# Performance work log

Measured on AMD Instinct MI355X. Metric: run time of the kernel, lower is better.

The kernel has to match this reference:

```python
import jax, jax.numpy as jnp
import numpy as np

# ---- config (matches init_kwargs) ----
GROUP_NUM = 2048
K_NEIGHBORS = 32
OUT_DIM = 192
SIGMA, BASELINE, SCALING, EPS = 0.26, 0.1, 10.0, 1e-6
ALPHA, BETA = 1000.0, 100.0
ADAPTIVE_RATIO = 0.5
IN_DIM = 3
ADAPTIVE_DIM = int(OUT_DIM * ADAPTIVE_RATIO)          # 96
FOURIER_DIM = OUT_DIM - ADAPTIVE_DIM                  # 96
FEAT_DIM_F = FOURIER_DIM // (IN_DIM * 2)              # 16
FEAT_DIM_A = int(np.ceil(ADAPTIVE_DIM / IN_DIM))      # 32
FEAT_NUM_A = FEAT_DIM_A * IN_DIM                      # 96
OUT_IDX = np.linspace(0, FEAT_NUM_A - 1, ADAPTIVE_DIM).astype(np.int64)


def setup_inputs() -> dict:
    key = jax.random.key(0)
    k1, k2, k3, k4 = jax.random.split(key, 4)
    xyz = jax.random.normal(k1, (4, 8192, 3), dtype=jnp.float32)
    x = jax.random.normal(k2, (4, 8192, 96), dtype=jnp.float32)
    bn_gamma = jax.random.uniform(k3, (192,), dtype=jnp.float32)
    bn_beta = jax.random.normal(k4, (192,), dtype=jnp.float32)
    return {"xyz": xyz, "x": x, "bn_gamma": bn_gamma, "bn_beta": bn_beta}


def _fps(xyz, m):
    """Farthest point sampling. xyz: [B,N,3] -> idx [B,m] (int32). Seed = index 0."""
    def single(pts):
        n = pts.shape[0]
        def step(carry, _):
            dists, last = carry
            d = jnp.sum((pts - pts[last]) ** 2, axis=-1)
            dists = jnp.minimum(dists, d)
            nxt = jnp.argmax(dists).astype(jnp.int32)
            return (dists, nxt), nxt
        init = (jnp.full((n,), 1e10, pts.dtype), jnp.array(0, jnp.int32))
        _, idxs = jax.lax.scan(step, init, None, length=m - 1)
        return jnp.concatenate([jnp.zeros((1,), jnp.int32), idxs])
    return jax.vmap(single)(xyz)


def _square_distance(src, dst):
    # src: [B,S,3], dst: [B,N,3] -> [B,S,N]
    d = -2.0 * jnp.einsum('bsc,bnc->bsn', src, dst)
    d += jnp.sum(src ** 2, -1)[:, :, None]
    d += jnp.sum(dst ** 2, -1)[:, None, :]
    return d


def _gather_knn(points, idx):
    # points: [B,N,C], idx: [B,G,K] -> [B,G,K,C]
    return jax.vmap(lambda p, i: p[i])(points, idx)


def _forward(xyz, x, bn_gamma, bn_beta):
    B, N, _ = xyz.shape
    G, K = GROUP_NUM, K_NEIGHBORS

    # ---- Grouper_seg ----
    fps_idx = _fps(xyz, G)                                   # [B,G]
    lc_xyz = jnp.take_along_axis(xyz, fps_idx[..., None], 1)  # [B,G,3]
    lc_x = jnp.take_along_axis(x, fps_idx[..., None], 1)      # [B,G,C]
    sqr = _square_distance(lc_xyz, xyz)                       # [B,G,N]
    knn_idx = jax.lax.top_k(-sqr, K)[1]                       # [B,G,K] smallest-k
    knn_xyz = _gather_knn(xyz, knn_idx)                       # [B,G,K,3]
    knn_x = _gather_knn(x, knn_idx)                           # [B,G,K,C]

    # ---- Aggregation_seg: local normalization ----
    mean_x = lc_x[:, :, None, :]
    std_x = jnp.std(knn_x - mean_x, ddof=1)
    mean_xyz = lc_xyz[:, :, None, :]
    std_xyz = jnp.std(knn_xyz - mean_xyz, ddof=1)
    knn_x = (knn_x - mean_x) / (std_x + 1e-5)
    knn_xyz_n = (knn_xyz - mean_xyz) / (std_xyz + 1e-5)       # [B,G,K,3]
    C = knn_x.shape[-1]
    knn_x = jnp.concatenate(
        [knn_x, jnp.broadcast_to(lc_x[:, :, None, :], (B, G, K, C))], axis=-1)  # [B,G,K,2C]
    knn_xyz_cf = jnp.transpose(knn_xyz_n, (0, 3, 1, 2))       # [B,3,G,K]
    knn_x_cf = jnp.transpose(knn_x, (0, 3, 1, 2))             # [B,OUT_DIM,G,K]

    # ---- PosE_Geo: fourier part ----
    feat_range = jnp.arange(FEAT_DIM_F, dtype=knn_xyz_cf.dtype)
    dim_embed = ALPHA ** (feat_range / FEAT_DIM_F)            # [F]
    div = BETA * knn_xyz_cf[..., None] / dim_embed            # [B,3,G,K,F]
    fourier = jnp.stack([jnp.sin(div), jnp.cos(div)], axis=-1)  # [B,3,G,K,F,2]
    fourier = fourier.reshape(B, IN_DIM, G, K, 2 * FEAT_DIM_F)
    fourier = jnp.transpose(fourier, (0, 1, 4, 2, 3)).reshape(B, FOURIER_DIM, G, K)

    # ---- AdaptiveEmbedding (parameterless, data-driven) ----
    x4 = knn_xyz_n                                            # [B,G,K,3]
    gstd = jnp.mean(jnp.std(x4.reshape(B, -1, IN_DIM), axis=1, ddof=1))
    sig = SIGMA * (1.0 + gstd) + EPS
    blend = jax.nn.sigmoid((gstd - BASELINE) * SCALING)
    feat_val = jnp.linspace(-1.0, 1.0, FEAT_DIM_A + 2)[1:-1]  # [Fa]
    z = (x4[..., None] - feat_val) / sig                      # [B,G,K,3,Fa]
    comb = blend * jnp.exp(-0.5 * z * z) + (1.0 - blend) * jnp.cos(z)
    ae = comb.reshape(B, G, K, FEAT_NUM_A)[..., OUT_IDX]      # [B,G,K,ADAPTIVE_DIM]
    ae_cf = jnp.transpose(ae, (0, 3, 1, 2))                   # [B,ADAPTIVE_DIM,G,K]

    pe = jnp.concatenate([fourier, ae_cf], axis=1)            # [B,OUT_DIM,G,K]
    knn_x_w = (knn_x_cf + pe) * pe

    # ---- Pooling_seg: max+mean pool, BatchNorm1d (train stats) + GELU ----
    lc = jnp.max(knn_x_w, -1) + jnp.mean(knn_x_w, -1)         # [B,OUT_DIM,G]
    mu = jnp.mean(lc, axis=(0, 2), keepdims=True)
    var = jnp.var(lc, axis=(0, 2), keepdims=True)
    y = (lc - mu) / jnp.sqrt(var + 1e-5)
    y = y * bn_gamma[None, :, None] + bn_beta[None, :, None]
    return jax.nn.gelu(y, approximate=False)


def reference(xyz, x, bn_gamma, bn_beta):
    return _forward(xyz, x, bn_gamma, bn_beta)
```

## Files before the change

kernel.cpp:

```cpp
#include <hip/hip_runtime.h>
#include <cstdint>
#include <math.h>

#define NPTS 8192
#define NB 4
#define NG 2048
#define NK 32
#define CIN 96
#define COUT 192

typedef float v2f __attribute__((ext_vector_type(2)));

__global__ __launch_bounds__(256) void setup_kernel(const float* __restrict__ xyz,
                                                    float* __restrict__ xs, float* __restrict__ ys,
                                                    float* __restrict__ zs, float* __restrict__ d2){
  int i = blockIdx.x*256 + threadIdx.x;
  if (i >= NB*NPTS) return;
  float x = xyz[3*i+0], y = xyz[3*i+1], z = xyz[3*i+2];
  xs[i]=x; ys[i]=y; zs[i]=z;
  d2[i] = __fadd_rn(__fadd_rn(__fmul_rn(x,x),__fmul_rn(y,y)),__fmul_rn(z,z));
}

__global__ __launch_bounds__(256,1) void fps_kernel(const float* __restrict__ xyz, int* __restrict__ fps_idx){
#pragma clang fp contract(off)
  extern __shared__ char smem[];
  float4* ctab = (float4*)smem;
  unsigned long long* slots = (unsigned long long*)(smem + NPTS*16);
  const int b = blockIdx.x;
  const int t = threadIdx.x;
  const float* base = xyz + (size_t)b*NPTS*3;
  v2f px[16], py[16], pz[16], D[16];
#pragma unroll
  for (int j=0;j<16;++j){
    int p0 = t + 512*j, p1 = p0 + 256;
    float x0=base[3*p0+0], y0=base[3*p0+1], z0=base[3*p0+2];
    float x1=base[3*p1+0], y1=base[3*p1+1], z1=base[3*p1+2];
    px[j]=(v2f){x0,x1}; py[j]=(v2f){y0,y1}; pz[j]=(v2f){z0,z1};
    D[j]=(v2f){1e10f,1e10f};
    ctab[p0] = make_float4(x0,y0,z0,0.f);
    ctab[p1] = make_float4(x1,y1,z1,0.f);
  }
  if (t<4) slots[t]=0ULL;
  if (t==0) fps_idx[b*NG]=0;
  __syncthreads();
  float lx=base[0], ly=base[1], lz=base[2];
  for (int it=0; it<NG-1; ++it){
    v2f bm = (v2f){-1.0f,-1.0f};
#pragma unroll
    for (int j=0;j<16;++j){
      v2f dx = px[j]-lx, dy = py[j]-ly, dz = pz[j]-lz;
      v2f s = (dx*dx + dy*dy) + dz*dz;
      v2f nd = __builtin_elementwise_min(D[j], s);
      D[j] = nd;
      bm = __builtin_elementwise_max(bm, nd);
    }
    float bd = fmaxf(bm.x, bm.y);
    int bj = 0;
#pragma unroll
    for (int j=15;j>=0;--j){
      if (D[j].y == bd) bj = 2*j+1;
      if (D[j].x == bd) bj = 2*j;
    }
    const int bp = t + (bj<<8);
    unsigned long long key = (((unsigned long long)__float_as_uint(bd))<<32)
                           | (unsigned long long)(unsigned)(~bp);
#pragma unroll
    for (int off=32; off>0; off>>=1){
      unsigned long long ok = __shfl_xor(key, off);
      if (ok > key) key = ok;
    }
    if ((t&63)==0) atomicMax(&slots[it&3], key);
    __syncthreads();
    unsigned long long wk = slots[it&3];
    if (t==0) slots[(it+2)&3] = 0ULL;
    int pw = (int)(~(unsigned)wk);
    float4 c = ctab[pw];
    lx=c.x; ly=c.y; lz=c.z;
    if (t==0) fps_idx[b*NG + it + 1] = pw;
  }
}

__device__ __forceinline__ bool lexlt(float ad, int ai, float bd, int bi){
  return (ad < bd) || ((ad == bd) && (ai < bi));
}
__device__ __forceinline__ void sort_desc(float& d, int& i, int lane){
#pragma unroll
  for (int k=2;k<=64;k<<=1){
#pragma unroll
    for (int j=k>>1;j>0;j>>=1){
      float od = __shfl_xor(d, j);
      int   oi = __shfl_xor(i, j);
      bool dirUp = (lane & k) != 0;
      bool lower = (lane & j) == 0;
      bool less  = lexlt(d,i,od,oi);
      bool keep  = (less == (lower == dirUp));
      if (!keep){ d=od; i=oi; }
    }
  }
}
__device__ __forceinline__ void merge_asc(float& d, int& i, int lane){
#pragma unroll
  for (int j=32;j>0;j>>=1){
    float od = __shfl_xor(d, j);
    int   oi = __shfl_xor(i, j);
    bool lower = (lane & j) == 0;
    bool less  = lexlt(d,i,od,oi);
    bool keep  = (less == lower);
    if (!keep){ d=od; i=oi; }
  }
}

__global__ __launch_bounds__(256) void knn_kernel(const float* __restrict__ xs, const float* __restrict__ ys,
                                                  const float* __restrict__ zs, const float* __restrict__ d2,
                                                  const int* __restrict__ fps_idx, int* __restrict__ knn_out){
  __shared__ float tx[256], ty[256], tz[256], td[256];
  const int tid = threadIdx.x;
  const int wid = tid>>6, lane = tid&63;
  const int pid = blockIdx.x*4 + wid;
  const int b = pid >> 11;
  const float* bx = xs + b*NPTS;
  const float* by = ys + b*NPTS;
  const float* bz = zs + b*NPTS;
  const float* bD = d2 + b*NPTS;
  const int fi = fps_idx[pid];
  const float ax = bx[fi], ay = by[fi], az = bz[fi];
  const float src2 = __fadd_rn(__fadd_rn(__fmul_rn(ax,ax),__fmul_rn(ay,ay)),__fmul_rn(az,az));
  float Ad = INFINITY; int Ai = 0x7fffffff;
  float tau_d = INFINITY; int tau_i = 0x7fffffff;
  for (int s=0; s<NPTS/256; ++s){
    __syncthreads();
    int gidx = s*256 + tid;
    tx[tid]=bx[gidx]; ty[tid]=by[gidx]; tz[tid]=bz[gidx]; td[tid]=bD[gidx];
    __syncthreads();
    float m0,m1,m2,m3; int i0,i1,i2,i3;
#define LOADJ(mj, ij, J) { int li = (J)*64 + lane; \
    float dot = __fadd_rn(__fadd_rn(__fmul_rn(ax,tx[li]),__fmul_rn(ay,ty[li])),__fmul_rn(az,tz[li])); \
    mj = __fadd_rn(__fadd_rn(__fmul_rn(-2.0f,dot), src2), td[li]); ij = s*256 + li; }
    LOADJ(m0,i0,0) LOADJ(m1,i1,1) LOADJ(m2,i2,2) LOADJ(m3,i3,3)
#undef LOADJ
    while (true){
      bool any = lexlt(m0,i0,tau_d,tau_i) || lexlt(m1,i1,tau_d,tau_i) ||
                 lexlt(m2,i2,tau_d,tau_i) || lexlt(m3,i3,tau_d,tau_i);
      if (__ballot(any) == 0ull) break;
      float cd = m0; int ci = i0; int sel = 0;
      if (lexlt(m1,i1,cd,ci)){ cd=m1; ci=i1; sel=1; }
      if (lexlt(m2,i2,cd,ci)){ cd=m2; ci=i2; sel=2; }
      if (lexlt(m3,i3,cd,ci)){ cd=m3; ci=i3; sel=3; }
      if      (sel==0) m0=INFINITY;
      else if (sel==1) m1=INFINITY;
      else if (sel==2) m2=INFINITY;
      else             m3=INFINITY;
      sort_desc(cd, ci, lane);
      if (lexlt(cd,ci,Ad,Ai)){ Ad=cd; Ai=ci; }
      merge_asc(Ad, Ai, lane);
      tau_d = __shfl(Ad, 31);
      tau_i = __shfl(Ai, 31);
    }
  }
  if (lane < NK) knn_out[pid*NK + lane] = Ai;
}

__global__ __launch_bounds__(256) void stats_kernel(const float* __restrict__ x, const float* __restrict__ xyz,
                                                    const int* __restrict__ fps_idx, const int* __restrict__ knn,
                                                    double* __restrict__ partials){
  const int tid=threadIdx.x, wid=tid>>6, lane=tid&63;
  const int pid = blockIdx.x*4 + wid;
  const int b = pid>>11;
  const int fi = fps_idx[pid];
  const float* xb = x + (size_t)b*NPTS*CIN;
  const float* zb = xyz + (size_t)b*NPTS*3;
  const float lc0 = xb[fi*CIN + lane];
  float lc1 = 0.f; if (lane<32) lc1 = xb[fi*CIN + 64 + lane];
  float czv = 0.f; if (lane<3)  czv = zb[fi*3 + lane];
  double s1=0.0, s2=0.0, a1=0.0, a2=0.0;
  for (int k=0;k<NK;++k){
    int idx = knn[pid*NK + k];
    float d0 = __fsub_rn(xb[idx*CIN + lane], lc0);
    s1 += (double)d0; s2 += (double)d0*(double)d0;
    if (lane<32){
      float d1 = __fsub_rn(xb[idx*CIN + 64 + lane], lc1);
      s1 += (double)d1; s2 += (double)d1*(double)d1;
    }
    if (lane<3){
      float w = __fsub_rn(zb[idx*3 + lane], czv);
      a1 += (double)w; a2 += (double)w*(double)w;
    }
  }
#pragma unroll
  for (int off=32; off>0; off>>=1){ s1 += __shfl_xor(s1,off); s2 += __shfl_xor(s2,off); }
  __shared__ double shx[4][2];
  __shared__ double shz[4][3][2];
  if (lane==0){ shx[wid][0]=s1; shx[wid][1]=s2; }
  if (lane<3){ shz[wid][lane][0]=a1; shz[wid][lane][1]=a2; }
  __syncthreads();
  if (tid==0){
    double u0=0,u1=0;
    for (int w=0;w<4;++w){ u0+=shx[w][0]; u1+=shx[w][1]; }
    double* outp = partials + (size_t)blockIdx.x*8;
    outp[0]=u0; outp[1]=u1;
    for (int axq=0; axq<3; ++axq){
      double v0=0,v1=0;
      for (int w=0;w<4;++w){ v0+=shz[w][axq][0]; v1+=shz[w][axq][1]; }
      outp[2+2*axq]=v0; outp[3+2*axq]=v1;
    }
  }
}

__global__ void finalize_kernel(const double* __restrict__ partials, float* __restrict__ scal){
  const int lane = threadIdx.x;
  double s1=0,s2=0;
  double z0a=0,z0b=0,z1a=0,z1b=0,z2a=0,z2b=0;
  for (int i=0;i<32;++i){
    const double* p = partials + (size_t)(lane*32+i)*8;
    s1+=p[0]; s2+=p[1];
    z0a+=p[2]; z0b+=p[3]; z1a+=p[4]; z1b+=p[5]; z2a+=p[6]; z2b+=p[7];
  }
#pragma unroll
  for (int off=32; off>0; off>>=1){ s1+=__shfl_xor(s1,off); s2+=__shfl_xor(s2,off); }
#pragma unroll
  for (int off=8; off>0; off>>=1){
    z0a+=__shfl_xor(z0a,off); z0b+=__shfl_xor(z0b,off);
    z1a+=__shfl_xor(z1a,off); z1b+=__shfl_xor(z1b,off);
    z2a+=__shfl_xor(z2a,off); z2b+=__shfl_xor(z2b,off);
  }
  __shared__ double zb[4][3][2];
  if ((lane&15)==0){
    int b = lane>>4;
    zb[b][0][0]=z0a; zb[b][0][1]=z0b;
    zb[b][1][0]=z1a; zb[b][1][1]=z1b;
    zb[b][2][0]=z2a; zb[b][2][1]=z2b;
  }
  __syncthreads();
  if (lane==0){
    double nx = (double)NB*NG*NK*CIN;
    double varx = (s2 - s1*s1/nx)/(nx-1.0);
    float stdx = (float)sqrt(varx);
    double t1=0,t2=0;
    for (int b=0;b<4;++b) for (int a=0;a<3;++a){ t1+=zb[b][a][0]; t2+=zb[b][a][1]; }
    double nz = (double)NB*NG*NK*3;
    double varz = (t2 - t1*t1/nz)/(nz-1.0);
    float stdz = (float)sqrt(varz);
    float sdiv = stdz + 1e-5f;
    double n2 = (double)NG*NK;
    double acc=0.0;
    for (int b=0;b<4;++b) for (int a=0;a<3;++a){
      double v = (zb[b][a][1] - zb[b][a][0]*zb[b][a][0]/n2)/(n2-1.0);
      acc += sqrt(v);
    }
    float gstd = (float)(acc/12.0) / sdiv;
    float sig = 0.26f*(1.0f+gstd) + 1e-6f;
    float blend = 1.0f/(1.0f + expf(-(gstd-0.1f)*10.0f));
    scal[0] = 1.0f/(stdx + 1e-5f);
    scal[1] = 1.0f/sdiv;
    scal[2] = 1.0f/sig;
    scal[3] = blend;
  }
}

__global__ __launch_bounds__(256) void main_kernel(const float* __restrict__ x, const float* __restrict__ xyz,
                                                   const int* __restrict__ fps_idx, const int* __restrict__ knn,
                                                   const float* __restrict__ scal, float* __restrict__ lc_out){
  const int tid=threadIdx.x, wid=tid>>6, lane=tid&63;
  const int pid = blockIdx.x*4 + wid;
  const int b = pid>>11, g = pid&2047;
  const float inv_x = scal[0], inv_z = scal[1], inv_sig = scal[2], blend = scal[3];
  const float omb = 1.0f - blend;
  const int fi = fps_idx[pid];
  const float* xb = x + (size_t)b*NPTS*CIN;
  const float* zb = xyz + (size_t)b*NPTS*3;
  const float cx = zb[fi*3+0], cy = zb[fi*3+1], cz = zb[fi*3+2];
  const float lcx0 = xb[fi*CIN + lane];
  const float lcx1 = (lane<32) ? xb[fi*CIN + 64 + lane] : xb[fi*CIN + lane - 32];
  const float lcx2 = xb[fi*CIN + 32 + lane];
  const int dim0 = lane>>5;
  const int rr0 = lane&31;
  const bool cos0 = rr0 & 1;
  const float bs0 = 100.0f / powf(1000.0f, (float)(rr0>>1) * (1.0f/16.0f));
  const bool cos1 = lane & 1;
  const float bs1 = 100.0f / powf(1000.0f, (float)((lane&31)>>1) * (1.0f/16.0f));
  const float fv1 = (float)(-1.0 + 2.0*(double)(lane-32+1)/33.0);
  const int dim2 = (32+lane)>>5;
  const int j2 = (32+lane)&31;
  const float fv2 = (float)(-1.0 + 2.0*(double)(j2+1)/33.0);

  float mx0=-INFINITY, mx1=-INFINITY, mx2=-INFINITY;
  float sm0=0.f, sm1=0.f, sm2=0.f;
  for (int k=0;k<NK;++k){
    const int idx = knn[pid*NK + k];
    const float p0 = zb[idx*3+0], p1 = zb[idx*3+1], p2v = zb[idx*3+2];
    const float xn0 = (p0-cx)*inv_z, xn1 = (p1-cy)*inv_z, xn2 = (p2v-cz)*inv_z;
    const float xk0 = xb[idx*CIN + lane];
    float xk1 = 0.f; if (lane<32) xk1 = xb[idx*CIN + 64 + lane];
    {
      float v = dim0 ? xn1 : xn0;
      float a = v * bs0;
      float pe = cos0 ? __cosf(a) : __sinf(a);
      float f = (xk0 - lcx0) * inv_x;
      float w = (f + pe) * pe;
      mx0 = fmaxf(mx0, w); sm0 += w;
    }
    {
      float pe, f;
      if (lane < 32){
        float a = xn2 * bs1;
        pe = cos1 ? __cosf(a) : __sinf(a);
        f = (xk1 - lcx1) * inv_x;
      } else {
        float zq = (xn0 - fv1) * inv_sig;
        pe = blend * __expf(-0.5f*zq*zq) + omb * __cosf(zq);
        f = lcx1;
      }
      float w = (f + pe) * pe;
      mx1 = fmaxf(mx1, w); sm1 += w;
    }
    {
      float v = (dim2==1) ? xn1 : xn2;
      float zq = (v - fv2) * inv_sig;
      float pe = blend * __expf(-0.5f*zq*zq) + omb * __cosf(zq);
      float w = (lcx2 + pe) * pe;
      mx2 = fmaxf(mx2, w); sm2 += w;
    }
  }
  const size_t obase = ((size_t)b*COUT)*NG + g;
  lc_out[obase + (size_t)lane*NG]       = mx0 + sm0*(1.0f/32.0f);
  lc_out[obase + (size_t)(64+lane)*NG]  = mx1 + sm1*(1.0f/32.0f);
  lc_out[obase + (size_t)(128+lane)*NG] = mx2 + sm2*(1.0f/32.0f);
}

__global__ __launch_bounds__(256) void bn_stats_kernel(const float* __restrict__ lc, float* __restrict__ bn){
  const int c = blockIdx.x, t = threadIdx.x, lane=t&63, wid=t>>6;
  double s1=0.0, s2=0.0;
  for (int i=t; i<NB*NG; i+=256){
    int b=i>>11, g=i&2047;
    float v = lc[((size_t)(b*COUT)+c)*NG + g];
    s1 += (double)v; s2 += (double)v*(double)v;
  }
#pragma unroll
  for (int off=32; off>0; off>>=1){ s1+=__shfl_xor(s1,off); s2+=__shfl_xor(s2,off); }
  __shared__ double sh1[4], sh2[4];
  if (lane==0){ sh1[wid]=s1; sh2[wid]=s2; }
  __syncthreads();
  if (t==0){
    double a=sh1[0]+sh1[1]+sh1[2]+sh1[3], q=sh2[0]+sh2[1]+sh2[2]+sh2[3];
    double n=(double)(NB*NG);
    double mu=a/n, var=q/n - mu*mu;
    bn[c]=(float)mu;
    bn[COUT+c]=(float)(1.0/sqrt(var + 1e-5));
  }
}

__global__ __launch_bounds__(256) void final_kernel(const float* __restrict__ bn, const float* __restrict__ gamma,
                                                    const float* __restrict__ beta, float* __restrict__ out){
  int i = blockIdx.x*256 + threadIdx.x;
  int c = (i >> 11) % COUT;
  float v = out[i];
  float y = (v - bn[c]) * bn[COUT + c];
  y = y*gamma[c] + beta[c];
  out[i] = y * 0.5f * (1.0f + erff(y * 0.70710678118654752f));
}

extern "C" void kernel_launch(void* const* d_in, const int* in_sizes, int n_in,
                              void* d_out, int out_size, void* d_ws, size_t ws_size,
                              hipStream_t stream){
  const float* xyz   = (const float*)d_in[0];
  const float* x     = (const float*)d_in[1];
  const float* gamma = (const float*)d_in[2];
  const float* beta  = (const float*)d_in[3];
  float* out = (float*)d_out;
  char* ws = (char*)d_ws;
  int*    fps  = (int*)   (ws + 0);
  int*    knn  = (int*)   (ws + 32768);
  float*  xs   = (float*) (ws + 1081344);
  float*  ys   = (float*) (ws + 1212416);
  float*  zs   = (float*) (ws + 1343488);
  float*  d2   = (float*) (ws + 1474560);
  double* parts= (double*)(ws + 1605632);
  float*  scal = (float*) (ws + 1736704);
  float*  bn   = (float*) (ws + 1736768);

  const int fps_lds = NPTS*16 + 4*8;
  static bool attr_set = false;
  (void)hipFuncSetAttribute(reinterpret_cast<const void*>(fps_kernel),
                            hipFuncAttributeMaxDynamicSharedMemorySize, fps_lds);

  setup_kernel   <<<dim3((NB*NPTS+255)/256), dim3(256), 0, stream>>>(xyz, xs, ys, zs, d2);
  fps_kernel     <<<dim3(NB),                dim3(256), fps_lds, stream>>>(xyz, fps);
  knn_kernel     <<<dim3(NB*NG/4),           dim3(256), 0, stream>>>(xs, ys, zs, d2, fps, knn);
  stats_kernel   <<<dim3(NB*NG/4),           dim3(256), 0, stream>>>(x, xyz, fps, knn, parts);
  finalize_kernel<<<dim3(1),                 dim3(64),  0, stream>>>(parts, scal);
  main_kernel    <<<dim3(NB*NG/4),           dim3(256), 0, stream>>>(x, xyz, fps, knn, scal, out);
  bn_stats_kernel<<<dim3(COUT),              dim3(256), 0, stream>>>(out, bn);
  final_kernel   <<<dim3((NB*COUT*NG)/256),  dim3(256), 0, stream>>>(bn, gamma, beta, out);
}
```

Before: 2.686 ms.

## Restructure FPS argmax with DPP wave reductions and per-wave LDS keys

The FPS kernel now runs 512 threads per block with 16 points per thread instead of 256 with 32, which halves the serial per-thread distance update. The 64-bit shuffle-based argmax is replaced by a DPP float max across the wave, then a DPP unsigned min over the winning indices. Each wave writes its key to a double-buffered LDS slot, and every thread reduces the 8 slots after the barrier, so the global-memory-style atomicMax and slot reset go away. The cost is a larger barrier group and an 8-entry LDS scan on every iteration of the sequential loop.

```diff
diff --git a/kernel.cpp b/kernel.cpp
--- a/kernel.cpp
+++ b/kernel.cpp
@@ -10,6 +10,7 @@
 #define COUT 192
 
 typedef float v2f __attribute__((ext_vector_type(2)));
+typedef unsigned long long ull;
 
 __global__ __launch_bounds__(256) void setup_kernel(const float* __restrict__ xyz,
                                                     float* __restrict__ xs, float* __restrict__ ys,
@@ -21,18 +22,40 @@
   d2[i] = __fadd_rn(__fadd_rn(__fmul_rn(x,x),__fmul_rn(y,y)),__fmul_rn(z,z));
 }
 
-__global__ __launch_bounds__(256,1) void fps_kernel(const float* __restrict__ xyz, int* __restrict__ fps_idx){
+template<int CTRL>
+__device__ __forceinline__ float dppmaxf(float v){
+  int o = __builtin_amdgcn_update_dpp(__float_as_int(v), __float_as_int(v), CTRL, 0xf, 0xf, false);
+  return fmaxf(v, __int_as_float(o));
+}
+template<int CTRL>
+__device__ __forceinline__ unsigned dppminu(unsigned v){
+  unsigned o = (unsigned)__builtin_amdgcn_update_dpp((int)v, (int)v, CTRL, 0xf, 0xf, false);
+  return (o < v) ? o : v;
+}
+__device__ __forceinline__ float wavemaxf(float v){
+  v = dppmaxf<0x111>(v); v = dppmaxf<0x112>(v); v = dppmaxf<0x114>(v);
+  v = dppmaxf<0x118>(v); v = dppmaxf<0x142>(v); v = dppmaxf<0x143>(v);
+  return v;
+}
+__device__ __forceinline__ unsigned waveminu(unsigned v){
+  v = dppminu<0x111>(v); v = dppminu<0x112>(v); v = dppminu<0x114>(v);
+  v = dppminu<0x118>(v); v = dppminu<0x142>(v); v = dppminu<0x143>(v);
+  return v;
+}
+
+__global__ __launch_bounds__(512,2) void fps_kernel(const float* __restrict__ xyz, int* __restrict__ fps_idx){
 #pragma clang fp contract(off)
   extern __shared__ char smem[];
   float4* ctab = (float4*)smem;
-  unsigned long long* slots = (unsigned long long*)(smem + NPTS*16);
+  ull* wavekeys = (ull*)(smem + NPTS*16);
   const int b = blockIdx.x;
   const int t = threadIdx.x;
+  const int w = t>>6, lane = t&63;
   const float* base = xyz + (size_t)b*NPTS*3;
-  v2f px[16], py[16], pz[16], D[16];
-#pragma unroll
-  for (int j=0;j<16;++j){
-    int p0 = t + 512*j, p1 = p0 + 256;
+  v2f px[8], py[8], pz[8], D[8];
+#pragma unroll
+  for (int j=0;j<8;++j){
+    int p0 = t + 1024*j, p1 = p0 + 512;
     float x0=base[3*p0+0], y0=base[3*p0+1], z0=base[3*p0+2];
     float x1=base[3*p1+0], y1=base[3*p1+1], z1=base[3*p1+2];
     px[j]=(v2f){x0,x1}; py[j]=(v2f){y0,y1}; pz[j]=(v2f){z0,z1};
@@ -40,14 +63,13 @@
     ctab[p0] = make_float4(x0,y0,z0,0.f);
     ctab[p1] = make_float4(x1,y1,z1,0.f);
   }
-  if (t<4) slots[t]=0ULL;
   if (t==0) fps_idx[b*NG]=0;
   __syncthreads();
   float lx=base[0], ly=base[1], lz=base[2];
   for (int it=0; it<NG-1; ++it){
     v2f bm = (v2f){-1.0f,-1.0f};
 #pragma unroll
-    for (int j=0;j<16;++j){
+    for (int j=0;j<8;++j){
       v2f dx = px[j]-lx, dy = py[j]-ly, dz = pz[j]-lz;
       v2f s = (dx*dx + dy*dy) + dz*dz;
       v2f nd = __builtin_elementwise_min(D[j], s);
@@ -55,28 +77,28 @@
       bm = __builtin_elementwise_max(bm, nd);
     }
     float bd = fmaxf(bm.x, bm.y);
-    int bj = 0;
-#pragma unroll
-    for (int j=15;j>=0;--j){
-      if (D[j].y == bd) bj = 2*j+1;
-      if (D[j].x == bd) bj = 2*j;
-    }
-    const int bp = t + (bj<<8);
-    unsigned long long key = (((unsigned long long)__float_as_uint(bd))<<32)
-                           | (unsigned long long)(unsigned)(~bp);
-#pragma unroll
-    for (int off=32; off>0; off>>=1){
-      unsigned long long ok = __shfl_xor(key, off);
-      if (ok > key) key = ok;
-    }
-    if ((t&63)==0) atomicMax(&slots[it&3], key);
+    float m = wavemaxf(bd);
+    float bdw = __int_as_float(__builtin_amdgcn_readlane(__float_as_int(m), 63));
+    unsigned li = 0xFFFFFFFFu;
+    if (bd == bdw){
+#pragma unroll
+      for (int j=7;j>=0;--j){
+        if (D[j].y == bdw) li = (unsigned)(t + (j<<10) + 512);
+        if (D[j].x == bdw) li = (unsigned)(t + (j<<10));
+      }
+    }
+    unsigned mn = waveminu(li);
+    if (lane==63)
+      wavekeys[(it&1)*8 + w] = (((ull)__float_as_uint(bdw))<<32) | (ull)(~mn);
     __syncthreads();
-    unsigned long long wk = slots[it&3];
-    if (t==0) slots[(it+2)&3] = 0ULL;
-    int pw = (int)(~(unsigned)wk);
+    const ull* wk = wavekeys + (it&1)*8;
+    ull k = wk[0];
+#pragma unroll
+    for (int q=1;q<8;++q){ ull o = wk[q]; if (o > k) k = o; }
+    unsigned pw = ~(unsigned)k;
     float4 c = ctab[pw];
     lx=c.x; ly=c.y; lz=c.z;
-    if (t==0) fps_idx[b*NG + it + 1] = pw;
+    if (t==0) fps_idx[b*NG + it + 1] = (int)pw;
   }
 }
 
@@ -378,13 +400,12 @@
   float*  scal = (float*) (ws + 1736704);
   float*  bn   = (float*) (ws + 1736768);
 
-  const int fps_lds = NPTS*16 + 4*8;
-  static bool attr_set = false;
+  const int fps_lds = NPTS*16 + 2*8*8;
   (void)hipFuncSetAttribute(reinterpret_cast<const void*>(fps_kernel),
                             hipFuncAttributeMaxDynamicSharedMemorySize, fps_lds);
 
   setup_kernel   <<<dim3((NB*NPTS+255)/256), dim3(256), 0, stream>>>(xyz, xs, ys, zs, d2);
-  fps_kernel     <<<dim3(NB),                dim3(256), fps_lds, stream>>>(xyz, fps);
+  fps_kernel     <<<dim3(NB),                dim3(512), fps_lds, stream>>>(xyz, fps);
   knn_kernel     <<<dim3(NB*NG/4),           dim3(256), 0, stream>>>(xs, ys, zs, d2, fps, knn);
   stats_kernel   <<<dim3(NB*NG/4),           dim3(256), 0, stream>>>(x, xyz, fps, knn, parts);
   finalize_kernel<<<dim3(1),                 dim3(64),  0, stream>>>(parts, scal);
```

After: 2.555 ms. -4.9%, faster.

## Rework FPS argmax reduction with packed keys, DPP wave max, and 512 threads

Applied to the files above, without the earlier changes.

The farthest point sampling kernel now runs 512 threads per block with 16 points each and drops the paired float vectors. Each point's distance is packed with a reversed index into a 64-bit key, so the per-thread argmax becomes a tree of integer maxes instead of a compare-then-search loop. The cross-lane step uses DPP row operations in place of shuffles. The shared atomicMax slot with its reset is replaced by double-buffered per-wave keys that every thread reduces after the barrier. The intent is a shorter serial critical path in each of the ~2047 iterations, at the cost of more 64-bit compares and a larger block to synchronise.

```diff
diff --git a/kernel.cpp b/kernel.cpp
--- a/kernel.cpp
+++ b/kernel.cpp
@@ -9,7 +9,7 @@
 #define CIN 96
 #define COUT 192
 
-typedef float v2f __attribute__((ext_vector_type(2)));
+typedef unsigned long long ull;
 
 __global__ __launch_bounds__(256) void setup_kernel(const float* __restrict__ xyz,
                                                     float* __restrict__ xs, float* __restrict__ ys,
@@ -21,62 +21,69 @@
   d2[i] = __fadd_rn(__fadd_rn(__fmul_rn(x,x),__fmul_rn(y,y)),__fmul_rn(z,z));
 }
 
-__global__ __launch_bounds__(256,1) void fps_kernel(const float* __restrict__ xyz, int* __restrict__ fps_idx){
+__device__ __forceinline__ ull umax64(ull a, ull b){ return (a>b)?a:b; }
+
+template<int CTRL>
+__device__ __forceinline__ ull dppmax64(ull v){
+  unsigned lo=(unsigned)v, hi=(unsigned)(v>>32);
+  unsigned olo=(unsigned)__builtin_amdgcn_update_dpp((int)lo,(int)lo,CTRL,0xf,0xf,false);
+  unsigned ohi=(unsigned)__builtin_amdgcn_update_dpp((int)hi,(int)hi,CTRL,0xf,0xf,false);
+  ull o=((ull)ohi<<32)|(ull)olo;
+  return (o>v)?o:v;
+}
+__device__ __forceinline__ ull wavemax64(ull v){
+  v=dppmax64<0x111>(v); v=dppmax64<0x112>(v); v=dppmax64<0x114>(v);
+  v=dppmax64<0x118>(v); v=dppmax64<0x142>(v); v=dppmax64<0x143>(v);
+  return v;
+}
+
+__global__ __launch_bounds__(512,2) void fps_kernel(const float* __restrict__ xyz, int* __restrict__ fps_idx){
 #pragma clang fp contract(off)
   extern __shared__ char smem[];
   float4* ctab = (float4*)smem;
-  unsigned long long* slots = (unsigned long long*)(smem + NPTS*16);
-  const int b = blockIdx.x;
-  const int t = threadIdx.x;
+  ull*    keys = (ull*)(smem + 131072);
+  const int b = blockIdx.x, t = threadIdx.x;
+  const int w = t>>6, lane = t&63;
   const float* base = xyz + (size_t)b*NPTS*3;
-  v2f px[16], py[16], pz[16], D[16];
+  float px[16], py[16], pz[16], D[16];
+  unsigned kc[16];
 #pragma unroll
   for (int j=0;j<16;++j){
-    int p0 = t + 512*j, p1 = p0 + 256;
-    float x0=base[3*p0+0], y0=base[3*p0+1], z0=base[3*p0+2];
-    float x1=base[3*p1+0], y1=base[3*p1+1], z1=base[3*p1+2];
-    px[j]=(v2f){x0,x1}; py[j]=(v2f){y0,y1}; pz[j]=(v2f){z0,z1};
-    D[j]=(v2f){1e10f,1e10f};
-    ctab[p0] = make_float4(x0,y0,z0,0.f);
-    ctab[p1] = make_float4(x1,y1,z1,0.f);
-  }
-  if (t<4) slots[t]=0ULL;
+    int p = t + 512*j;
+    float x=base[3*p+0], y=base[3*p+1], z=base[3*p+2];
+    px[j]=x; py[j]=y; pz[j]=z;
+    D[j]=1e10f;
+    kc[j]=8191u-(unsigned)p;
+    ctab[p] = make_float4(x,y,z,0.f);
+  }
   if (t==0) fps_idx[b*NG]=0;
   __syncthreads();
   float lx=base[0], ly=base[1], lz=base[2];
   for (int it=0; it<NG-1; ++it){
-    v2f bm = (v2f){-1.0f,-1.0f};
+    ull K[16];
 #pragma unroll
     for (int j=0;j<16;++j){
-      v2f dx = px[j]-lx, dy = py[j]-ly, dz = pz[j]-lz;
-      v2f s = (dx*dx + dy*dy) + dz*dz;
-      v2f nd = __builtin_elementwise_min(D[j], s);
-      D[j] = nd;
-      bm = __builtin_elementwise_max(bm, nd);
-    }
-    float bd = fmaxf(bm.x, bm.y);
-    int bj = 0;
-#pragma unroll
-    for (int j=15;j>=0;--j){
-      if (D[j].y == bd) bj = 2*j+1;
-      if (D[j].x == bd) bj = 2*j;
-    }
-    const int bp = t + (bj<<8);
-    unsigned long long key = (((unsigned long long)__float_as_uint(bd))<<32)
-                           | (unsigned long long)(unsigned)(~bp);
-#pragma unroll
-    for (int off=32; off>0; off>>=1){
-      unsigned long long ok = __shfl_xor(key, off);
-      if (ok > key) key = ok;
-    }
-    if ((t&63)==0) atomicMax(&slots[it&3], key);
+      float dx=px[j]-lx, dy=py[j]-ly, dz=pz[j]-lz;
+      float d=(dx*dx+dy*dy)+dz*dz;
+      float Dn=fminf(D[j],d);
+      D[j]=Dn;
+      K[j]=(((ull)__float_as_uint(Dn))<<32)|(ull)kc[j];
+    }
+#pragma unroll
+    for (int s=8;s>0;s>>=1)
+#pragma unroll
+      for (int j=0;j<16;++j) if (j<s) K[j]=umax64(K[j],K[j+s]);
+    ull P = wavemax64(K[0]);
+    if (lane==63) keys[(it&1)*8 + w] = P;
     __syncthreads();
-    unsigned long long wk = slots[it&3];
-    if (t==0) slots[(it+2)&3] = 0ULL;
-    int pw = (int)(~(unsigned)wk);
-    float4 c = ctab[pw];
-    lx=c.x; ly=c.y; lz=c.z;
-    if (t==0) fps_idx[b*NG + it + 1] = pw;
+    const ull* kk = keys + (it&1)*8;
+    ull k0=umax64(kk[0],kk[1]), k1=umax64(kk[2],kk[3]);
+    ull k2=umax64(kk[4],kk[5]), k3=umax64(kk[6],kk[7]);
+    ull k = umax64(umax64(k0,k1),umax64(k2,k3));
+    unsigned pw = 8191u - (unsigned)(k & 0xffffffffu);
+    float4 c4 = ctab[pw];
+    lx=c4.x; ly=c4.y; lz=c4.z;
+    if (t==0) fps_idx[b*NG + it + 1] = (int)pw;
   }
 }
 
@@ -378,13 +385,12 @@
   float*  scal = (float*) (ws + 1736704);
   float*  bn   = (float*) (ws + 1736768);
 
-  const int fps_lds = NPTS*16 + 4*8;
-  static bool attr_set = false;
+  const int fps_lds = 131072 + 128;
   (void)hipFuncSetAttribute(reinterpret_cast<const void*>(fps_kernel),
                             hipFuncAttributeMaxDynamicSharedMemorySize, fps_lds);
 
   setup_kernel   <<<dim3((NB*NPTS+255)/256), dim3(256), 0, stream>>>(xyz, xs, ys, zs, d2);
-  fps_kernel     <<<dim3(NB),                dim3(256), fps_lds, stream>>>(xyz, fps);
+  fps_kernel     <<<dim3(NB),                dim3(512), fps_lds, stream>>>(xyz, fps);
   knn_kernel     <<<dim3(NB*NG/4),           dim3(256), 0, stream>>>(xs, ys, zs, d2, fps, knn);
   stats_kernel   <<<dim3(NB*NG/4),           dim3(256), 0, stream>>>(x, xyz, fps, knn, parts);
   finalize_kernel<<<dim3(1),                 dim3(64),  0, stream>>>(parts, scal);
```

After: 2.452 ms. 1.1x faster.
